# Performance work log

Hardware: AMD Instinct MI355X
Metric: run time of the kernel (lower is better)

Reference implementation:

```python
import jax, jax.numpy as jnp
import numpy as np

# Config (matches init_kwargs + Mamba2 defaults: expand=2, headdim=64, ngroups=1)
B_, C_IN, T, H, W = 4, 23, 8, 128, 128
P = 4
DM = 256
D_STATE = 16
D_CONV = 4
EXPAND = 2
D_INNER = EXPAND * DM            # 512
HEADDIM = 64
NHEADS = D_INNER // HEADDIM      # 8
CONV_DIM = D_INNER + 2 * D_STATE # 544 (ngroups=1)
D_IN_PROJ = 2 * D_INNER + 2 * D_STATE + NHEADS


def setup_inputs() -> dict:
    key = jax.random.key(0)
    ks = jax.random.split(key, 12)
    s = lambda k, shape, sc: (jax.random.normal(k, shape, jnp.float32) * sc)
    x = jax.random.normal(ks[0], (B_, C_IN, T, H, W), jnp.float32)
    patch_w = s(ks[1], (DM, C_IN, P, P), 0.05)       # Conv3d weight, depth-1 dim squeezed
    patch_b = s(ks[2], (DM,), 0.02)
    W_in = s(ks[3], (DM, D_IN_PROJ), 0.05)           # in_proj (bias=False)
    conv_w = s(ks[4], (CONV_DIM, D_CONV), 0.2)       # depthwise conv1d weight
    conv_b = s(ks[5], (CONV_DIM,), 0.02)
    dt_bias = jnp.log(jnp.expm1(jnp.exp(jax.random.uniform(ks[6], (NHEADS,), jnp.float32, jnp.log(1e-3), jnp.log(1e-1)))))
    A_log = jnp.log(jnp.arange(1, NHEADS + 1, dtype=jnp.float32))
    D_param = jnp.ones((NHEADS,), jnp.float32)
    norm_w = jnp.ones((D_INNER,), jnp.float32)
    W_out = s(ks[7], (D_INNER, DM), 0.05)            # out_proj (bias=False)
    unembed_w = s(ks[8], (DM, C_IN, P, P), 0.05)     # ConvTranspose3d weight (in,out,1,p,p)
    unembed_b = s(ks[9], (C_IN,), 0.02)
    return {"x": x, "patch_w": patch_w, "patch_b": patch_b, "W_in": W_in,
            "conv_w": conv_w, "conv_b": conv_b, "dt_bias": dt_bias, "A_log": A_log,
            "D_param": D_param, "norm_w": norm_w, "W_out": W_out,
            "unembed_w": unembed_w, "unembed_b": unembed_b}


def reference(x, patch_w, patch_b, W_in, conv_w, conv_b, dt_bias, A_log,
              D_param, norm_w, W_out, unembed_w, unembed_b):
    B, C, Tt, Hh, Ww = x.shape
    p = patch_w.shape[-1]
    Hp, Wp = Hh // p, Ww // p
    L = Tt * Hp * Wp
    # --- Conv3d patch embed (kernel (1,p,p), stride (1,p,p)) == non-overlapping patchify ---
    xr = x.reshape(B, C, Tt, Hp, p, Wp, p)
    emb = jnp.einsum('bcthiwj,dcij->bthwd', xr, patch_w) + patch_b  # [B,T,Hp,Wp,D]
    xs = emb.reshape(B, L, DM)
    # --- Mamba2 ---
    zxbcdt = xs @ W_in                                 # [B,L,2*d_inner+2*d_state+nheads]
    z = zxbcdt[:, :, :D_INNER]
    xBC = zxbcdt[:, :, D_INNER:D_INNER + CONV_DIM]
    dt = zxbcdt[:, :, D_INNER + CONV_DIM:]             # [B,L,nheads]
    # causal depthwise conv1d + silu
    xp = jnp.pad(xBC, ((0, 0), (D_CONV - 1, 0), (0, 0)))
    conv_out = conv_b + sum(xp[:, k:k + L, :] * conv_w[:, k] for k in range(D_CONV))
    xBC = jax.nn.silu(conv_out)
    xh = xBC[:, :, :D_INNER].reshape(B, L, NHEADS, HEADDIM)
    Bm = xBC[:, :, D_INNER:D_INNER + D_STATE]          # [B,L,N] (ngroups=1)
    Cm = xBC[:, :, D_INNER + D_STATE:]                 # [B,L,N]
    dt = jax.nn.softplus(dt + dt_bias)                 # [B,L,H]
    A = -jnp.exp(A_log)                                # [H]
    dA = jnp.exp(dt * A)                               # [B,L,H]
    xdt = xh * dt[..., None]                           # [B,L,H,P]
    # selective state-space scan: h_t = dA_t h_{t-1} + (dt_t x_t) B_t^T ; y_t = h_t C_t
    def step(h, inp):
        dA_t, xdt_t, B_t, C_t = inp
        h = dA_t[..., None, None] * h + jnp.einsum('bhp,bn->bhpn', xdt_t, B_t)
        y = jnp.einsum('bhpn,bn->bhp', h, C_t)
        return h, y
    inps = (dA.transpose(1, 0, 2), xdt.transpose(1, 0, 2, 3),
            Bm.transpose(1, 0, 2), Cm.transpose(1, 0, 2))
    h0 = jnp.zeros((B, NHEADS, HEADDIM, D_STATE), xs.dtype)
    _, ys = jax.lax.scan(step, h0, inps)               # [L,B,H,P]
    y = ys.transpose(1, 0, 2, 3) + D_param[None, None, :, None] * xh
    y = y.reshape(B, L, D_INNER)
    # gated RMSNorm (norm_before_gate=False): rmsnorm(y * silu(z)) * w
    yg = y * jax.nn.silu(z)
    y = yg * jax.lax.rsqrt(jnp.mean(yg * yg, axis=-1, keepdims=True) + 1e-5) * norm_w
    out_seq = y @ W_out                                # [B,L,DM]
    # --- ConvTranspose3d unembed (kernel (1,p,p), stride (1,p,p)) == un-patchify ---
    outp = out_seq.reshape(B, Tt, Hp, Wp, DM)
    un = jnp.einsum('bthwd,dcij->bcthiwj', outp, unembed_w)
    out = un.reshape(B, C, Tt, Hh, Ww) + unembed_b[None, :, None, None, None]
    return out + x
```

## Files before the change

kernel.cpp:

```cpp
#include <hip/hip_runtime.h>
#include <hip/hip_bf16.h>
#include <cstdint>
#include <cstddef>

#define B_N       4
#define C_INCH    23
#define T_N       8
#define W_IMG     128
#define L_SEQ     8192
#define BLROWS    32768
#define DM_       256
#define D_INNER_  512
#define CONV_DIM_ 544
#define D_PROJ    1064
#define KPATCH    368
#define QCH       64
#define NCH       128
#define RECW      48
#define PFD       8

typedef unsigned short ushort_t;
typedef unsigned int uint_t;
typedef __attribute__((ext_vector_type(8))) short short8;
typedef __attribute__((ext_vector_type(4))) float f32x4;

__device__ __forceinline__ float b2f(ushort_t u) {
    union { float f; uint_t u; } v; v.u = ((uint_t)u) << 16; return v.f;
}
__device__ __forceinline__ ushort_t f2b(float f) {
    union { float f; uint_t u; } v; v.f = f;
    uint_t r = v.u + 0x7fffu + ((v.u >> 16) & 1u);
    return (ushort_t)(r >> 16);
}

__device__ __forceinline__ void gload_lds16(const ushort_t* g, ushort_t* l) {
    __builtin_amdgcn_global_load_lds(
        (const __attribute__((address_space(1))) unsigned int*)g,
        (__attribute__((address_space(3))) unsigned int*)l, 16, 0, 0);
}

__global__ void k_transcast(const float* __restrict__ src, ushort_t* __restrict__ dst,
                            int K, int N, const float* __restrict__ rscale) {
    int n = blockIdx.x;
    for (int k = threadIdx.x; k < K; k += 256) {
        float v = 0.f;
        if (n < N) {
            v = src[(size_t)k * N + n];
            if (rscale) v *= rscale[k];
        }
        dst[(size_t)n * K + k] = f2b(v);
    }
}

__global__ void k_castpad(const float* __restrict__ src, ushort_t* __restrict__ dst) {
    int d = blockIdx.x; int k = threadIdx.x;
    dst[d * 384 + k] = (k < KPATCH) ? f2b(src[d * KPATCH + k]) : (ushort_t)0;
}

__global__ void __launch_bounds__(256) k_im2col(const float* __restrict__ x,
                                                ushort_t* __restrict__ Aim) {
    int hp = blockIdx.x, t = blockIdx.y, b = blockIdx.z;
    int tid = threadIdx.x;
    int half = tid >> 7, q = tid & 127;
    int wp = q >> 2, j = q & 3;
    size_t rowbase = (size_t)b * L_SEQ + t * 1024 + hp * 32;
    #pragma unroll
    for (int it = 0; it < 2; ++it) {
        int idx = it * 256 + tid;
        int wpz = idx >> 4, kz = KPATCH + (idx & 15);
        Aim[(rowbase + wpz) * 384 + kz] = 0;
    }
    for (int s2 = 0; s2 < 46; ++s2) {
        int seg = s2 * 2 + half;
        int c = seg >> 2, i = seg & 3;
        float v = x[(((size_t)(b * C_INCH + c) * T_N + t) << 14) + (size_t)(hp * 4 + i) * W_IMG + q];
        Aim[(rowbase + wp) * 384 + c * 16 + i * 4 + j] = f2b(v);
    }
}

template <int K, int N, bool CBF>
__global__ void __launch_bounds__(256) k_mgemm(const ushort_t* __restrict__ A, const int lda,
                                               const ushort_t* __restrict__ Wt,
                                               void* __restrict__ Cv, const int ldc, const int coff,
                                               const float* __restrict__ bias,
                                               const float* __restrict__ rowscale) {
    __shared__ ushort_t Al[128 * 64];
    __shared__ ushort_t Bl[128 * 64];
    const int tid = threadIdx.x;
    const int w = tid >> 6, lane = tid & 63;
    const int wr = w >> 1, wc = w & 1;
    const int rowbase = blockIdx.y * 128;
    const int colbase = blockIdx.x * 128;
    const int g = lane >> 4, r = lane & 15;

    f32x4 acc[4][4];
    #pragma unroll
    for (int i = 0; i < 4; ++i)
        #pragma unroll
        for (int j = 0; j < 4; ++j) acc[i][j] = (f32x4){0.f, 0.f, 0.f, 0.f};

    for (int k0 = 0; k0 < K; k0 += 64) {
        __syncthreads();
        #pragma unroll
        for (int it = 0; it < 4; ++it) {
            int s = it * 256 + (w << 6) + lane;
            int row = s >> 3;
            int c16 = (s & 7) ^ (row & 7);
            gload_lds16(A + (size_t)(rowbase + row) * lda + k0 + c16 * 8,
                        &Al[(size_t)(it * 256 + (w << 6)) * 8]);
        }
        #pragma unroll
        for (int it = 0; it < 4; ++it) {
            int s = it * 256 + (w << 6) + lane;
            int row = s >> 3;
            int c16 = (s & 7) ^ (row & 7);
            gload_lds16(Wt + (size_t)(colbase + row) * K + k0 + c16 * 8,
                        &Bl[(size_t)(it * 256 + (w << 6)) * 8]);
        }
        __syncthreads();

        short8 af[2][4], bf[2][4];
        #pragma unroll
        for (int ks = 0; ks < 2; ++ks)
            #pragma unroll
            for (int mi = 0; mi < 4; ++mi) {
                int row = (wr << 6) + (mi << 4) + r;
                int c16 = ((ks << 2) | g) ^ (row & 7);
                af[ks][mi] = *(const short8*)&Al[(size_t)((row << 3) + c16) * 8];
            }
        #pragma unroll
        for (int ks = 0; ks < 2; ++ks)
            #pragma unroll
            for (int ni = 0; ni < 4; ++ni) {
                int row = (wc << 6) + (ni << 4) + r;
                int c16 = ((ks << 2) | g) ^ (row & 7);
                bf[ks][ni] = *(const short8*)&Bl[(size_t)((row << 3) + c16) * 8];
            }
        #pragma unroll
        for (int ks = 0; ks < 2; ++ks)
            #pragma unroll
            for (int mi = 0; mi < 4; ++mi)
                #pragma unroll
                for (int ni = 0; ni < 4; ++ni)
                    acc[mi][ni] = __builtin_amdgcn_mfma_f32_16x16x32_bf16(
                        af[ks][mi], bf[ks][ni], acc[mi][ni], 0, 0, 0);
    }

    #pragma unroll
    for (int mi = 0; mi < 4; ++mi) {
        int rw = rowbase + (wr << 6) + (mi << 4) + (g << 2);
        float s0 = 1.f, s1 = 1.f, s2 = 1.f, s3 = 1.f;
        if (rowscale) { s0 = rowscale[rw]; s1 = rowscale[rw+1]; s2 = rowscale[rw+2]; s3 = rowscale[rw+3]; }
        #pragma unroll
        for (int ni = 0; ni < 4; ++ni) {
            int col = colbase + (wc << 6) + (ni << 4) + r;
            if (col < N) {
                float bv = bias ? bias[col] : 0.f;
                f32x4 v = acc[mi][ni];
                float vr[4] = {v[0]*s0 + bv, v[1]*s1 + bv, v[2]*s2 + bv, v[3]*s3 + bv};
                #pragma unroll
                for (int j = 0; j < 4; ++j) {
                    size_t cidx = (size_t)(rw + j) * ldc + coff + col;
                    if (CBF) ((ushort_t*)Cv)[cidx] = f2b(vr[j]);
                    else     ((float*)Cv)[cidx]   = vr[j];
                }
            }
        }
    }
}

__global__ void __launch_bounds__(256) k_conv(const ushort_t* __restrict__ xbcdt,
                                              const float* __restrict__ cw,
                                              const float* __restrict__ cb,
                                              const float* __restrict__ dtb,
                                              const float* __restrict__ alog,
                                              ushort_t* __restrict__ xbc,
                                              float* __restrict__ brec) {
    int tid = threadIdx.x;
    int rb = blockIdx.x * 8;
    int srb = rb & (L_SEQ - 1);
    #pragma unroll
    for (int it = 0; it < 3; ++it) {
        int ch = it * 256 + tid;
        if (ch >= 552) break;
        if (ch < CONV_DIM_) {
            float w0 = cw[ch * 4 + 0], w1 = cw[ch * 4 + 1];
            float w2 = cw[ch * 4 + 2], w3 = cw[ch * 4 + 3];
            float bias = cb[ch];
            float win[11];
            #pragma unroll
            for (int j = 0; j < 11; ++j) {
                int sj = srb + j - 3;
                win[j] = (sj >= 0) ? b2f(xbcdt[(size_t)(rb + j - 3) * 640 + ch]) : 0.f;
            }
            #pragma unroll
            for (int r = 0; r < 8; ++r) {
                float acc = bias + win[r] * w0 + win[r + 1] * w1 + win[r + 2] * w2 + win[r + 3] * w3;
                float s = acc / (1.f + __expf(-acc));
                size_t row = rb + r;
                if (ch < 512) xbc[row * 512 + ch] = f2b(s);
                else          brec[row * RECW + (ch - 512)] = s;
            }
        } else {
            int h = ch - CONV_DIM_;
            float A = -__expf(alog[h]);
            float db = dtb[h];
            #pragma unroll
            for (int r = 0; r < 8; ++r) {
                size_t row = rb + r;
                float v = b2f(xbcdt[row * 640 + ch]) + db;
                float sp = (v > 20.f) ? v : log1pf(__expf(v));
                brec[row * RECW + 32 + h] = __expf(sp * A);
                brec[row * RECW + 40 + h] = sp;
            }
        }
    }
}

__global__ void __launch_bounds__(256) k_scan1(const ushort_t* __restrict__ xbc,
                                               const float* __restrict__ brec,
                                               float* __restrict__ sbuf,
                                               float* __restrict__ cdf) {
    __shared__ float rec[QCH * RECW];
    int c = blockIdx.x, b = blockIdx.z;
    int tid = threadIdx.x;
    int h = blockIdx.y * 4 + (tid >> 6);
    int p = tid & 63;
    int off = h * 64 + p;
    size_t row0 = (size_t)b * L_SEQ + (size_t)c * QCH;

    {
        const float4* src = (const float4*)(brec + row0 * RECW);
        float4* dst = (float4*)rec;
        #pragma unroll
        for (int i = 0; i < 3; ++i) dst[i * 256 + tid] = src[i * 256 + tid];
    }

    float st[16];
    #pragma unroll
    for (int n = 0; n < 16; ++n) st[n] = 0.f;
    float cd = 1.f;
    float xh[PFD];
    #pragma unroll
    for (int j = 0; j < PFD; ++j) xh[j] = b2f(xbc[(row0 + j) * 512 + off]);
    __syncthreads();

    for (int s0 = 0; s0 < QCH; s0 += PFD) {
        float xhn[PFD];
        #pragma unroll
        for (int j = 0; j < PFD; ++j)
            xhn[j] = b2f(xbc[(row0 + s0 + PFD + j) * 512 + off]);
        #pragma unroll
        for (int j = 0; j < PFD; ++j) {
            const float* r = rec + (s0 + j) * RECW;
            float da  = r[32 + h];
            float dtt = r[40 + h];
            float xdt = xh[j] * dtt;
            const float4* B4 = (const float4*)r;
            #pragma unroll
            for (int q = 0; q < 4; ++q) {
                float4 Bv = B4[q];
                st[q*4+0] = da * st[q*4+0] + xdt * Bv.x;
                st[q*4+1] = da * st[q*4+1] + xdt * Bv.y;
                st[q*4+2] = da * st[q*4+2] + xdt * Bv.z;
                st[q*4+3] = da * st[q*4+3] + xdt * Bv.w;
            }
            cd *= da;
        }
        #pragma unroll
        for (int j = 0; j < PFD; ++j) xh[j] = xhn[j];
    }
    size_t base = (size_t)((b * 8 + h) * NCH + c) * 1024 + p * 16;
    #pragma unroll
    for (int q = 0; q < 4; ++q)
        *(float4*)&sbuf[base + q * 4] = make_float4(st[q*4], st[q*4+1], st[q*4+2], st[q*4+3]);
    if (p == 0) cdf[(b * 8 + h) * NCH + c] = cd;
}

__global__ void __launch_bounds__(256) k_chain(const float* __restrict__ sbuf,
                                               const float* __restrict__ cdf,
                                               float* __restrict__ hin) {
    int h = blockIdx.x, b = blockIdx.y;
    int tid = threadIdx.x;
    float4 H = make_float4(0.f, 0.f, 0.f, 0.f);
    size_t base = (size_t)((b * 8 + h) * NCH) * 1024;
    for (int c = 0; c < NCH; ++c) {
        *(float4*)&hin[base + (size_t)c * 1024 + tid * 4] = H;
        float cdfv = cdf[(b * 8 + h) * NCH + c];
        float4 S = *(const float4*)&sbuf[base + (size_t)c * 1024 + tid * 4];
        H.x = cdfv * H.x + S.x;
        H.y = cdfv * H.y + S.y;
        H.z = cdfv * H.z + S.z;
        H.w = cdfv * H.w + S.w;
    }
}

__global__ void __launch_bounds__(512) k_scan2(const ushort_t* __restrict__ xbc,
                                               const ushort_t* __restrict__ z_bf,
                                               const float* __restrict__ brec,
                                               const float* __restrict__ Dp,
                                               const float* __restrict__ hin,
                                               ushort_t* __restrict__ yg_out) {
    __shared__ float rec[QCH * RECW];
    int c = blockIdx.x, b = blockIdx.y;
    int tid = threadIdx.x;
    int h = tid >> 6, p = tid & 63;
    int off = h * 64 + p;
    size_t row0 = (size_t)b * L_SEQ + (size_t)c * QCH;

    {
        const float4* src = (const float4*)(brec + row0 * RECW);
        float4* dst = (float4*)rec;
        dst[tid] = src[tid];
        if (tid < 256) dst[512 + tid] = src[512 + tid];
    }

    float st[16];
    const float4* H = (const float4*)&hin[(size_t)((b * 8 + h) * NCH + c) * 1024 + p * 16];
    #pragma unroll
    for (int q = 0; q < 4; ++q) {
        float4 Hv = H[q];
        st[q*4+0] = Hv.x; st[q*4+1] = Hv.y; st[q*4+2] = Hv.z; st[q*4+3] = Hv.w;
    }
    float Dh = Dp[h];
    float xh[PFD], zz[PFD];
    #pragma unroll
    for (int j = 0; j < PFD; ++j) {
        xh[j] = b2f(xbc[(row0 + j) * 512 + off]);
        zz[j] = b2f(z_bf[(row0 + j) * 512 + off]);
    }
    __syncthreads();

    for (int s0 = 0; s0 < QCH; s0 += PFD) {
        float xhn[PFD], zzn[PFD];
        #pragma unroll
        for (int j = 0; j < PFD; ++j) {
            size_t rn = row0 + s0 + PFD + j;
            xhn[j] = b2f(xbc[rn * 512 + off]);
            zzn[j] = b2f(z_bf[rn * 512 + off]);
        }
        #pragma unroll
        for (int j = 0; j < PFD; ++j) {
            const float* r = rec + (s0 + j) * RECW;
            float da  = r[32 + h];
            float dtt = r[40 + h];
            float xdt = xh[j] * dtt;
            const float4* B4 = (const float4*)r;
            const float4* C4 = (const float4*)(r + 16);
            float d0 = 0.f, d1 = 0.f, d2 = 0.f, d3 = 0.f;
            #pragma unroll
            for (int q = 0; q < 4; ++q) {
                float4 Bv = B4[q];
                float4 Cv = C4[q];
                st[q*4+0] = da * st[q*4+0] + xdt * Bv.x;
                st[q*4+1] = da * st[q*4+1] + xdt * Bv.y;
                st[q*4+2] = da * st[q*4+2] + xdt * Bv.z;
                st[q*4+3] = da * st[q*4+3] + xdt * Bv.w;
                d0 += st[q*4+0] * Cv.x;
                d1 += st[q*4+1] * Cv.y;
                d2 += st[q*4+2] * Cv.z;
                d3 += st[q*4+3] * Cv.w;
            }
            float y = (d0 + d1) + (d2 + d3) + Dh * xh[j];
            float ygv = y * (zz[j] / (1.f + __expf(-zz[j])));
            yg_out[(row0 + s0 + j) * 512 + off] = f2b(ygv);
        }
        #pragma unroll
        for (int j = 0; j < PFD; ++j) { xh[j] = xhn[j]; zz[j] = zzn[j]; }
    }
}

__global__ void __launch_bounds__(256) k_rsum(const ushort_t* __restrict__ yg,
                                              float* __restrict__ scale) {
    int wid = threadIdx.x >> 6, lane = threadIdx.x & 63;
    int row = blockIdx.x * 4 + wid;
    short8 v = *(const short8*)&yg[(size_t)row * 512 + lane * 8];
    float s = 0.f;
    #pragma unroll
    for (int j = 0; j < 8; ++j) {
        float f = b2f((ushort_t)v[j]);
        s += f * f;
    }
    #pragma unroll
    for (int off = 32; off >= 1; off >>= 1) s += __shfl_xor(s, off);
    if (lane == 0) scale[row] = rsqrtf(s * (1.f / 512.f) + 1e-5f);
}

__global__ void __launch_bounds__(256) k_scatter(const ushort_t* __restrict__ tmp,
                                                 const float* __restrict__ ub,
                                                 const float* __restrict__ xin,
                                                 float* __restrict__ out) {
    int tid = threadIdx.x;
    int w = tid & 127;
    int h = (blockIdx.x << 1) | (tid >> 7);
    int c = blockIdx.y >> 3, t = blockIdx.y & 7;
    int b = blockIdx.z;
    size_t row = (size_t)b * L_SEQ + t * 1024 + (h >> 2) * 32 + (w >> 2);
    int kk = c * 16 + (h & 3) * 4 + (w & 3);
    size_t oidx = (((size_t)(b * C_INCH + c) * T_N + t) << 14) + (size_t)h * W_IMG + w;
    out[oidx] = b2f(tmp[row * KPATCH + kk]) + ub[c] + xin[oidx];
}

extern "C" void kernel_launch(void* const* d_in, const int* in_sizes, int n_in,
                              void* d_out, int out_size, void* d_ws, size_t ws_size,
                              hipStream_t stream) {
    const float* x       = (const float*)d_in[0];
    const float* patch_w = (const float*)d_in[1];
    const float* patch_b = (const float*)d_in[2];
    const float* W_in    = (const float*)d_in[3];
    const float* conv_w  = (const float*)d_in[4];
    const float* conv_b  = (const float*)d_in[5];
    const float* dt_bias = (const float*)d_in[6];
    const float* A_log   = (const float*)d_in[7];
    const float* D_param = (const float*)d_in[8];
    const float* norm_w  = (const float*)d_in[9];
    const float* W_out   = (const float*)d_in[10];
    const float* unemb_w = (const float*)d_in[11];
    const float* unemb_b = (const float*)d_in[12];
    float* out = (float*)d_out;

    char* p = (char*)d_ws;
    ushort_t* scratch = (ushort_t*)p; p += (size_t)BLROWS * 384 * 2;
    float* scale= (float*)p;   p += (size_t)BLROWS * 4;
    float* cdf  = (float*)p;   p += (size_t)32 * NCH * 4;
    float* sbuf = (float*)p;   p += (size_t)32 * NCH * 1024 * 4;
    float* hin  = (float*)p;   p += (size_t)32 * NCH * 1024 * 4;
    float* brec = (float*)p;   p += (size_t)BLROWS * RECW * 4;
    ushort_t* Wt_p   = (ushort_t*)p; p += (size_t)256 * 384 * 2;
    ushort_t* Wt_in  = (ushort_t*)p; p += (size_t)1152 * 256 * 2;
    ushort_t* Wt_out = (ushort_t*)p; p += (size_t)256 * 512 * 2;
    ushort_t* Wt_un  = (ushort_t*)p; p += (size_t)384 * 256 * 2;
    ushort_t* xs     = (ushort_t*)p; p += (size_t)BLROWS * DM_ * 2;
    ushort_t* xbc    = (ushort_t*)p; p += (size_t)BLROWS * 512 * 2;
    ushort_t* z_bf   = (ushort_t*)p; p += (size_t)BLROWS * 512 * 2;
    ushort_t* xbcdt  = (ushort_t*)p; p += (size_t)BLROWS * 640 * 2;
    size_t need = (size_t)(p - (char*)d_ws);
    if (ws_size < need) return;

    ushort_t* Aim = scratch;
    ushort_t* tmp = scratch;
    ushort_t* yg  = xbcdt;

    k_castpad<<<256, 384, 0, stream>>>(patch_w, Wt_p);
    k_transcast<<<1152, 256, 0, stream>>>(W_in, Wt_in, 256, 1064, nullptr);
    k_transcast<<<256, 256, 0, stream>>>(W_out, Wt_out, 512, 256, norm_w);
    k_transcast<<<384, 256, 0, stream>>>(unemb_w, Wt_un, 256, 368, nullptr);

    k_im2col<<<dim3(32, 8, 4), 256, 0, stream>>>(x, Aim);
    k_mgemm<384, 256, true><<<dim3(2, 256), 256, 0, stream>>>(Aim, 384, Wt_p, xs, 256, 0, patch_b, nullptr);

    k_mgemm<256, 512, true><<<dim3(4, 256), 256, 0, stream>>>(xs, 256, Wt_in, z_bf, 512, 0, nullptr, nullptr);
    k_mgemm<256, 552, true><<<dim3(5, 256), 256, 0, stream>>>(xs, 256, Wt_in + (size_t)512 * 256, xbcdt, 640, 0, nullptr, nullptr);

    k_conv<<<BLROWS / 8, 256, 0, stream>>>(xbcdt, conv_w, conv_b, dt_bias, A_log, xbc, brec);

    k_scan1<<<dim3(NCH, 2, 4), 256, 0, stream>>>(xbc, brec, sbuf, cdf);
    k_chain<<<dim3(8, 4), 256, 0, stream>>>(sbuf, cdf, hin);
    k_scan2<<<dim3(NCH, 4), 512, 0, stream>>>(xbc, z_bf, brec, D_param, hin, yg);
    k_rsum<<<BLROWS / 4, 256, 0, stream>>>(yg, scale);

    k_mgemm<512, 256, true><<<dim3(2, 256), 256, 0, stream>>>(yg, 512, Wt_out, xs, DM_, 0, nullptr, scale);

    k_mgemm<256, 368, true><<<dim3(3, 256), 256, 0, stream>>>(xs, 256, Wt_un, tmp, KPATCH, 0, nullptr, nullptr);

    k_scatter<<<dim3(64, 184, 4), 256, 0, stream>>>(tmp, unemb_b, x, out);
}
```

Baseline: 275.5 us.

## Fuse im2col into patch GEMM and RMSNorm row-sum into out-proj GEMM

The im2col kernel is removed and the patch-embed GEMM now reads x directly, converting float4 patches to bf16 into LDS. The separate row-sum-of-squares kernel is removed as well: the out-projection GEMM accumulates squared A-fragment values per row and computes the RMSNorm scale in its epilogue. This drops two launches and the round-trips through the Aim and scale buffers. In exchange the A loads in the patch GEMM become synchronous register loads with no async LDS copy, and extra ALU work is added inside the out-proj main loop.

```diff
diff --git a/kernel.cpp b/kernel.cpp
--- a/kernel.cpp
+++ b/kernel.cpp
@@ -57,33 +57,10 @@
     dst[d * 384 + k] = (k < KPATCH) ? f2b(src[d * KPATCH + k]) : (ushort_t)0;
 }
 
-__global__ void __launch_bounds__(256) k_im2col(const float* __restrict__ x,
-                                                ushort_t* __restrict__ Aim) {
-    int hp = blockIdx.x, t = blockIdx.y, b = blockIdx.z;
-    int tid = threadIdx.x;
-    int half = tid >> 7, q = tid & 127;
-    int wp = q >> 2, j = q & 3;
-    size_t rowbase = (size_t)b * L_SEQ + t * 1024 + hp * 32;
-    #pragma unroll
-    for (int it = 0; it < 2; ++it) {
-        int idx = it * 256 + tid;
-        int wpz = idx >> 4, kz = KPATCH + (idx & 15);
-        Aim[(rowbase + wpz) * 384 + kz] = 0;
-    }
-    for (int s2 = 0; s2 < 46; ++s2) {
-        int seg = s2 * 2 + half;
-        int c = seg >> 2, i = seg & 3;
-        float v = x[(((size_t)(b * C_INCH + c) * T_N + t) << 14) + (size_t)(hp * 4 + i) * W_IMG + q];
-        Aim[(rowbase + wp) * 384 + c * 16 + i * 4 + j] = f2b(v);
-    }
-}
-
-template <int K, int N, bool CBF>
-__global__ void __launch_bounds__(256) k_mgemm(const ushort_t* __restrict__ A, const int lda,
+__global__ void __launch_bounds__(256) k_pgemm(const float* __restrict__ x,
                                                const ushort_t* __restrict__ Wt,
-                                               void* __restrict__ Cv, const int ldc, const int coff,
-                                               const float* __restrict__ bias,
-                                               const float* __restrict__ rowscale) {
+                                               ushort_t* __restrict__ Cv,
+                                               const float* __restrict__ bias) {
     __shared__ ushort_t Al[128 * 64];
     __shared__ ushort_t Bl[128 * 64];
     const int tid = threadIdx.x;
@@ -92,12 +69,108 @@
     const int rowbase = blockIdx.y * 128;
     const int colbase = blockIdx.x * 128;
     const int g = lane >> 4, r = lane & 15;
+    const int b  = rowbase >> 13;
+    const int t  = (rowbase >> 10) & 7;
+    const int hp0 = (rowbase >> 5) & 31;
 
     f32x4 acc[4][4];
     #pragma unroll
     for (int i = 0; i < 4; ++i)
         #pragma unroll
         for (int j = 0; j < 4; ++j) acc[i][j] = (f32x4){0.f, 0.f, 0.f, 0.f};
+
+    for (int it = 0; it < 6; ++it) {
+        int k0 = it * 64;
+        __syncthreads();
+        #pragma unroll
+        for (int i2 = 0; i2 < 4; ++i2) {
+            int s = i2 * 256 + (w << 6) + lane;
+            int row = s >> 3;
+            int c16 = (s & 7) ^ (row & 7);
+            gload_lds16(Wt + (size_t)(colbase + row) * 384 + k0 + c16 * 8,
+                        &Bl[(size_t)(i2 * 256 + (w << 6)) * 8]);
+        }
+        #pragma unroll
+        for (int i2 = 0; i2 < 8; ++i2) {
+            int idx = i2 * 256 + tid;
+            int row = idx >> 4, kq = idx & 15;
+            int c = (k0 >> 4) + (kq >> 2);
+            int i = kq & 3;
+            uint_t u0 = 0, u1 = 0;
+            if (c < C_INCH) {
+                int hp = hp0 + (row >> 5), wp = row & 31;
+                const float4 v = *(const float4*)&x[(((size_t)(b * C_INCH + c) * T_N + t) << 14)
+                                                    + (size_t)(hp * 4 + i) * W_IMG + wp * 4];
+                u0 = (uint_t)f2b(v.x) | ((uint_t)f2b(v.y) << 16);
+                u1 = (uint_t)f2b(v.z) | ((uint_t)f2b(v.w) << 16);
+            }
+            int slot = (row << 3) + ((kq >> 1) ^ (row & 7));
+            *(uint2*)&Al[(size_t)slot * 8 + (kq & 1) * 4] = make_uint2(u0, u1);
+        }
+        __syncthreads();
+
+        short8 af[2][4], bf[2][4];
+        #pragma unroll
+        for (int ks = 0; ks < 2; ++ks)
+            #pragma unroll
+            for (int mi = 0; mi < 4; ++mi) {
+                int row = (wr << 6) + (mi << 4) + r;
+                int c16 = ((ks << 2) | g) ^ (row & 7);
+                af[ks][mi] = *(const short8*)&Al[(size_t)((row << 3) + c16) * 8];
+            }
+        #pragma unroll
+        for (int ks = 0; ks < 2; ++ks)
+            #pragma unroll
+            for (int ni = 0; ni < 4; ++ni) {
+                int row = (wc << 6) + (ni << 4) + r;
+                int c16 = ((ks << 2) | g) ^ (row & 7);
+                bf[ks][ni] = *(const short8*)&Bl[(size_t)((row << 3) + c16) * 8];
+            }
+        #pragma unroll
+        for (int ks = 0; ks < 2; ++ks)
+            #pragma unroll
+            for (int mi = 0; mi < 4; ++mi)
+                #pragma unroll
+                for (int ni = 0; ni < 4; ++ni)
+                    acc[mi][ni] = __builtin_amdgcn_mfma_f32_16x16x32_bf16(
+                        af[ks][mi], bf[ks][ni], acc[mi][ni], 0, 0, 0);
+    }
+
+    #pragma unroll
+    for (int mi = 0; mi < 4; ++mi) {
+        int rw = rowbase + (wr << 6) + (mi << 4) + (g << 2);
+        #pragma unroll
+        for (int ni = 0; ni < 4; ++ni) {
+            int col = colbase + (wc << 6) + (ni << 4) + r;
+            float bv = bias[col];
+            f32x4 v = acc[mi][ni];
+            #pragma unroll
+            for (int j = 0; j < 4; ++j)
+                Cv[(size_t)(rw + j) * DM_ + col] = f2b(v[j] + bv);
+        }
+    }
+}
+
+template <int K, int N, bool CBF, bool ASCALE>
+__global__ void __launch_bounds__(256) k_mgemm(const ushort_t* __restrict__ A, const int lda,
+                                               const ushort_t* __restrict__ Wt,
+                                               void* __restrict__ Cv, const int ldc, const int coff,
+                                               const float* __restrict__ bias) {
+    __shared__ ushort_t Al[128 * 64];
+    __shared__ ushort_t Bl[128 * 64];
+    const int tid = threadIdx.x;
+    const int w = tid >> 6, lane = tid & 63;
+    const int wr = w >> 1, wc = w & 1;
+    const int rowbase = blockIdx.y * 128;
+    const int colbase = blockIdx.x * 128;
+    const int g = lane >> 4, r = lane & 15;
+
+    f32x4 acc[4][4];
+    #pragma unroll
+    for (int i = 0; i < 4; ++i)
+        #pragma unroll
+        for (int j = 0; j < 4; ++j) acc[i][j] = (f32x4){0.f, 0.f, 0.f, 0.f};
+    float rs[4] = {0.f, 0.f, 0.f, 0.f};
 
     for (int k0 = 0; k0 < K; k0 += 64) {
         __syncthreads();
@@ -136,6 +209,17 @@
                 int c16 = ((ks << 2) | g) ^ (row & 7);
                 bf[ks][ni] = *(const short8*)&Bl[(size_t)((row << 3) + c16) * 8];
             }
+        if (ASCALE) {
+            #pragma unroll
+            for (int ks = 0; ks < 2; ++ks)
+                #pragma unroll
+                for (int mi = 0; mi < 4; ++mi)
+                    #pragma unroll
+                    for (int e = 0; e < 8; ++e) {
+                        float v = b2f((ushort_t)af[ks][mi][e]);
+                        rs[mi] += v * v;
+                    }
+        }
         #pragma unroll
         for (int ks = 0; ks < 2; ++ks)
             #pragma unroll
@@ -149,20 +233,27 @@
     #pragma unroll
     for (int mi = 0; mi < 4; ++mi) {
         int rw = rowbase + (wr << 6) + (mi << 4) + (g << 2);
-        float s0 = 1.f, s1 = 1.f, s2 = 1.f, s3 = 1.f;
-        if (rowscale) { s0 = rowscale[rw]; s1 = rowscale[rw+1]; s2 = rowscale[rw+2]; s3 = rowscale[rw+3]; }
+        float sj[4] = {1.f, 1.f, 1.f, 1.f};
+        if (ASCALE) {
+            float s = rs[mi];
+            s += __shfl_xor(s, 16);
+            s += __shfl_xor(s, 32);
+            float sc = rsqrtf(s * (1.f / 512.f) + 1e-5f);
+            #pragma unroll
+            for (int j = 0; j < 4; ++j) sj[j] = __shfl(sc, 4 * g + j);
+        }
         #pragma unroll
         for (int ni = 0; ni < 4; ++ni) {
             int col = colbase + (wc << 6) + (ni << 4) + r;
             if (col < N) {
                 float bv = bias ? bias[col] : 0.f;
                 f32x4 v = acc[mi][ni];
-                float vr[4] = {v[0]*s0 + bv, v[1]*s1 + bv, v[2]*s2 + bv, v[3]*s3 + bv};
                 #pragma unroll
                 for (int j = 0; j < 4; ++j) {
                     size_t cidx = (size_t)(rw + j) * ldc + coff + col;
-                    if (CBF) ((ushort_t*)Cv)[cidx] = f2b(vr[j]);
-                    else     ((float*)Cv)[cidx]   = vr[j];
+                    float vr = v[j] * sj[j] + bv;
+                    if (CBF) ((ushort_t*)Cv)[cidx] = f2b(vr);
+                    else     ((float*)Cv)[cidx]   = vr;
                 }
             }
         }
@@ -368,22 +459,6 @@
         #pragma unroll
         for (int j = 0; j < PFD; ++j) { xh[j] = xhn[j]; zz[j] = zzn[j]; }
     }
-}
-
-__global__ void __launch_bounds__(256) k_rsum(const ushort_t* __restrict__ yg,
-                                              float* __restrict__ scale) {
-    int wid = threadIdx.x >> 6, lane = threadIdx.x & 63;
-    int row = blockIdx.x * 4 + wid;
-    short8 v = *(const short8*)&yg[(size_t)row * 512 + lane * 8];
-    float s = 0.f;
-    #pragma unroll
-    for (int j = 0; j < 8; ++j) {
-        float f = b2f((ushort_t)v[j]);
-        s += f * f;
-    }
-    #pragma unroll
-    for (int off = 32; off >= 1; off >>= 1) s += __shfl_xor(s, off);
-    if (lane == 0) scale[row] = rsqrtf(s * (1.f / 512.f) + 1e-5f);
 }
 
 __global__ void __launch_bounds__(256) k_scatter(const ushort_t* __restrict__ tmp,
@@ -421,7 +496,6 @@
 
     char* p = (char*)d_ws;
     ushort_t* scratch = (ushort_t*)p; p += (size_t)BLROWS * 384 * 2;
-    float* scale= (float*)p;   p += (size_t)BLROWS * 4;
     float* cdf  = (float*)p;   p += (size_t)32 * NCH * 4;
     float* sbuf = (float*)p;   p += (size_t)32 * NCH * 1024 * 4;
     float* hin  = (float*)p;   p += (size_t)32 * NCH * 1024 * 4;
@@ -437,7 +511,6 @@
     size_t need = (size_t)(p - (char*)d_ws);
     if (ws_size < need) return;
 
-    ushort_t* Aim = scratch;
     ushort_t* tmp = scratch;
     ushort_t* yg  = xbcdt;
 
@@ -446,22 +519,20 @@
     k_transcast<<<256, 256, 0, stream>>>(W_out, Wt_out, 512, 256, norm_w);
     k_transcast<<<384, 256, 0, stream>>>(unemb_w, Wt_un, 256, 368, nullptr);
 
-    k_im2col<<<dim3(32, 8, 4), 256, 0, stream>>>(x, Aim);
-    k_mgemm<384, 256, true><<<dim3(2, 256), 256, 0, stream>>>(Aim, 384, Wt_p, xs, 256, 0, patch_b, nullptr);
-
-    k_mgemm<256, 512, true><<<dim3(4, 256), 256, 0, stream>>>(xs, 256, Wt_in, z_bf, 512, 0, nullptr, nullptr);
-    k_mgemm<256, 552, true><<<dim3(5, 256), 256, 0, stream>>>(xs, 256, Wt_in + (size_t)512 * 256, xbcdt, 640, 0, nullptr, nullptr);
+    k_pgemm<<<dim3(2, 256), 256, 0, stream>>>(x, Wt_p, xs, patch_b);
+
+    k_mgemm<256, 512, true, false><<<dim3(4, 256), 256, 0, stream>>>(xs, 256, Wt_in, z_bf, 512, 0, nullptr);
+    k_mgemm<256, 552, true, false><<<dim3(5, 256), 256, 0, stream>>>(xs, 256, Wt_in + (size_t)512 * 256, xbcdt, 640, 0, nullptr);
 
     k_conv<<<BLROWS / 8, 256, 0, stream>>>(xbcdt, conv_w, conv_b, dt_bias, A_log, xbc, brec);
 
     k_scan1<<<dim3(NCH, 2, 4), 256, 0, stream>>>(xbc, brec, sbuf, cdf);
     k_chain<<<dim3(8, 4), 256, 0, stream>>>(sbuf, cdf, hin);
     k_scan2<<<dim3(NCH, 4), 512, 0, stream>>>(xbc, z_bf, brec, D_param, hin, yg);
-    k_rsum<<<BLROWS / 4, 256, 0, stream>>>(yg, scale);
-
-    k_mgemm<512, 256, true><<<dim3(2, 256), 256, 0, stream>>>(yg, 512, Wt_out, xs, DM_, 0, nullptr, scale);
-
-    k_mgemm<256, 368, true><<<dim3(3, 256), 256, 0, stream>>>(xs, 256, Wt_un, tmp, KPATCH, 0, nullptr, nullptr);
+
+    k_mgemm<512, 256, true, true><<<dim3(2, 256), 256, 0, stream>>>(yg, 512, Wt_out, xs, DM_, 0, nullptr);
+
+    k_mgemm<256, 368, true, false><<<dim3(3, 256), 256, 0, stream>>>(xs, 256, Wt_un, tmp, KPATCH, 0, nullptr);
 
     k_scatter<<<dim3(64, 184, 4), 256, 0, stream>>>(tmp, unemb_b, x, out);
 }
```

Result: faster. 259.6 us (-5.8%).
